# Optimization experiments

Measured on AMD Instinct MI355X. Metric: run time of the kernel, lower is better.

Reference implementation:

```python
import jax, jax.numpy as jnp
import numpy as np

B, T, N = 32, 64, 2048
HID, HEADS, DH, BOT, MAX_LAG = 256, 8, 32, 64, 7


def setup_inputs() -> dict:
    key = jax.random.key(0)
    ks = jax.random.split(key, 12)
    def nrm(k, shape, s=0.05):
        return jax.random.normal(k, shape, jnp.float32) * s
    # delay logits init as in the module: log(softmaxed exp decay)
    w = np.exp(-np.arange(MAX_LAG + 1) / 3.0)
    w = w / w.sum()
    delay_logits = jnp.asarray(np.log(w + 1e-8), jnp.float32)
    # row-normalized adjacency prior (done in __init__ of the module)
    adj_raw = jax.random.uniform(ks[0], (N, N), jnp.float32)
    adj_prior = adj_raw / (adj_raw.sum(-1, keepdims=True) + 1e-8)
    return {
        "x": jax.random.normal(ks[1], (B, T, N), jnp.float32),
        "features": jax.random.normal(ks[2], (B, N, HID), jnp.float32),
        "delay_logits": delay_logits,
        "w_dp": nrm(ks[3], (1, HID)), "b_dp": jnp.zeros((HID,), jnp.float32),
        "w_qkv_low": nrm(ks[4], (HID, 3 * BOT)), "b_qkv_low": jnp.zeros((3 * BOT,), jnp.float32),
        "w_qkv_high": nrm(ks[5], (3 * BOT, 3 * HID)), "b_qkv_high": jnp.zeros((3 * HID,), jnp.float32),
        "w_out_low": nrm(ks[6], (HID, BOT)), "b_out_low": jnp.zeros((BOT,), jnp.float32),
        "w_out_high": nrm(ks[7], (BOT, HID)), "b_out_high": jnp.zeros((HID,), jnp.float32),
        "adj_prior": adj_prior,
        "geo_weight": jnp.array([0.3], jnp.float32),
        "ln_gamma": jnp.ones((HID,), jnp.float32),
        "ln_beta": jnp.zeros((HID,), jnp.float32),
    }


def reference(x, features, delay_logits, w_dp, b_dp,
              w_qkv_low, b_qkv_low, w_qkv_high, b_qkv_high,
              w_out_low, b_out_low, w_out_high, b_out_high,
              adj_prior, geo_weight, ln_gamma, ln_beta):
    # --- delay-weighted signal (generation interval) ---
    dw = jax.nn.softmax(delay_logits)                      # [max_lag+1]
    taus = min(MAX_LAG + 1, T)                              # static
    x_lags = jnp.flip(x, axis=1)[:, :taus]                  # [B,taus,N], lag tau = x[:, -(tau+1)]
    delayed = jnp.einsum('t,btn->bn', dw[:taus], x_lags)    # [B,N]
    delay_feat = delayed[:, :, None] * w_dp[0] + b_dp       # Linear(1, hidden)
    combined = features + 0.1 * delay_feat                  # [B,N,HID]

    # --- low-rank QKV ---
    qkv = (combined @ w_qkv_low + b_qkv_low) @ w_qkv_high + b_qkv_high  # [B,N,3*HID]
    q, k, v = jnp.split(qkv, 3, axis=-1)
    def to_heads(t):
        return t.reshape(B, N, HEADS, DH).transpose(0, 2, 1, 3)  # [B,H,N,dh]
    q, k, v = to_heads(q), to_heads(k), to_heads(v)

    # --- linear attention (elu+1 feature map, O(N)) ---
    qf = jax.nn.elu(q) + 1.0
    kf = jax.nn.elu(k) + 1.0
    kv = jnp.einsum('bhnd,bhne->bhde', kf, v)               # [B,H,dh,dh]
    k_sum = kf.sum(axis=2) + 1e-8                           # [B,H,dh]
    num = jnp.einsum('bhnd,bhde->bhne', qf, kv)             # [B,H,N,dh]
    den = jnp.einsum('bhnd,bhd->bhn', qf, k_sum)[..., None] + 1e-8
    attended = num / den

    # --- geo-adjacency blend ---
    gb = jax.nn.sigmoid(geo_weight[0])
    v_geo = jnp.einsum('nm,bhmd->bhnd', adj_prior, v)       # dense graph mixing
    attended = (1.0 - gb) * attended + gb * v_geo

    attended = attended.transpose(0, 2, 1, 3).reshape(B, N, HID)
    # dropout is identity in eval mode
    out = (attended @ w_out_low + b_out_low) @ w_out_high + b_out_high

    # --- residual + LayerNorm ---
    y = out + features
    mu = y.mean(-1, keepdims=True)
    var = ((y - mu) ** 2).mean(-1, keepdims=True)
    return (y - mu) / jnp.sqrt(var + 1e-5) * ln_gamma + ln_beta
```

## Files before the change

kernel.cpp:

```cpp
#include <hip/hip_runtime.h>
#include <hip/hip_bf16.h>
#include <stdint.h>

typedef unsigned short u16;
typedef float f4v __attribute__((ext_vector_type(4)));
typedef short s8v __attribute__((ext_vector_type(8)));


__device__ __forceinline__ float bf2f(u16 u) {
  union { float f; uint32_t i; } x; x.i = ((uint32_t)u) << 16; return x.f;
}
__device__ __forceinline__ u16 f2bf(float f) {
  uint32_t u = __float_as_uint(f);
  u = (u + 0x7FFFu + ((u >> 16) & 1u)) >> 16;
  return (u16)u;
}
__device__ __forceinline__ uint32_t pk2(float a, float b) {
  return (uint32_t)f2bf(a) | ((uint32_t)f2bf(b) << 16);
}
__device__ __forceinline__ void gload16(const void* g, void* l) {
  __builtin_amdgcn_global_load_lds((const __attribute__((address_space(1))) void*)g,
                                   (__attribute__((address_space(3))) void*)l, 16, 0, 0);
}

__global__ __launch_bounds__(256) void prep_all_k(
    const float* __restrict__ x, const float* __restrict__ dlog,
    const float* __restrict__ w_dp, const float* __restrict__ b_dp,
    const float* __restrict__ wql, const float* __restrict__ bql,
    const float* __restrict__ wqh, const float* __restrict__ wol,
    const float* __restrict__ bqh,
    float* __restrict__ wl_d, float* __restrict__ bl_p, float* __restrict__ delayed,
    u16* __restrict__ wqlT, u16* __restrict__ wqhT, u16* __restrict__ wvlT,
    float* __restrict__ cvl) {
  const int bid = blockIdx.x, t = threadIdx.x;
  if (bid < 256) {
    float mx = dlog[0];
#pragma unroll
    for (int i = 1; i < 8; ++i) mx = fmaxf(mx, dlog[i]);
    float w8[8], ssum = 0.f;
#pragma unroll
    for (int i = 0; i < 8; ++i) { w8[i] = __expf(dlog[i] - mx); ssum += w8[i]; }
    float inv = 1.f / ssum;
    int r = bid * 256 + t;
    int b = r >> 11, n = r & 2047;
    const float* xb = x + (size_t)b * 64 * 2048;
    float acc = 0.f;
#pragma unroll
    for (int tau = 0; tau < 8; ++tau) acc += w8[tau] * inv * xb[(size_t)(63 - tau) * 2048 + n];
    delayed[r] = acc;
  } else if (bid < 512) {
    int n = bid - 256;
    wqlT[(size_t)n * 256 + t] = f2bf(n < 192 ? wql[(size_t)t * 192 + n] : 0.f);
  } else if (bid < 1280) {
    int n = bid - 512;
    if (t < 192) wqhT[(size_t)n * 192 + t] = f2bf(wqh[(size_t)t * 768 + n]);
  } else if (bid < 1408) {
    int d = bid - 1280;
    __shared__ float wolc[256];
    if (d < 64) wolc[t] = wol[(size_t)t * 64 + d];
    __syncthreads();
    if (t < 192) {
      float s = 0.f;
      if (d < 64) {
        const float* wr = wqh + (size_t)t * 768 + 512;
        for (int c = 0; c < 256; ++c) s = fmaf(wr[c], wolc[c], s);
      }
      wvlT[(size_t)d * 192 + t] = f2bf(s);
    }
    if (t == 0 && d < 64) {
      float s = 0.f;
      for (int c = 0; c < 256; ++c) s = fmaf(bqh[512 + c], wolc[c], s);
      cvl[d] = s;
    }
  } else {
    if (t < 192) {
      float s1 = 0.f, s2 = 0.f;
      for (int k = 0; k < 256; ++k) {
        float w = wql[k * 192 + t];
        s1 += w_dp[k] * w;
        s2 += b_dp[k] * w;
      }
      wl_d[t] = 0.1f * s1;
      bl_p[t] = bql[t] + 0.1f * s2;
    }
  }
}

struct MArgs {
  const u16* A;
  const float* Af32;
  const u16* Bt;
  const float* delayed; const float* wl_d; const float* bl_p;
  const float* bqh;
  const float* cvl;
  u16* low; u16* qf; u16* kf; u16* v; u16* vpt;
  u16* geopart;
};

enum { GLOW = 0, GQKV = 1, GGEO = 2, GVP = 3 };

template <int MODE>
__global__ __launch_bounds__(256) void mgemm_k(MArgs ma) {
  constexpr int KLOOP = (MODE == GLOW) ? 256 : (MODE == GQKV) ? 192 :
                        (MODE == GGEO) ? 512 : 192;
  constexpr int LDA = (MODE == GLOW) ? 256 : (MODE == GGEO) ? 2048 : 192;
  constexpr int LDB = (MODE == GLOW) ? 256 : (MODE == GGEO) ? 2048 : 192;

  __shared__ __align__(16) u16 Al[128 * 64];
  __shared__ __align__(16) u16 Bl[128 * 64];

  const int t = threadIdx.x;
  const int l = t & 63, w = t >> 6;
  const int wm = w >> 1, wn = w & 1;

  int ct, rt, bz = 0;
  if constexpr (MODE == GGEO) {
    int lin = blockIdx.x + 16 * blockIdx.y + 256 * blockIdx.z;
    int xcd = lin & 7, idx = lin >> 3;
    ct = idx & 15;
    int pid = xcd * 8 + (idx >> 4);
    rt = pid & 15;
    bz = pid >> 4;
  } else {
    constexpr int NCT = (MODE == GLOW) ? 2 : (MODE == GQKV) ? 6 : 1;
    int lin = blockIdx.x + NCT * blockIdx.y;
    int xcd = lin & 7, idx = lin >> 3;
    ct = idx % NCT; rt = xcd * 64 + idx / NCT;
  }
  const int kbase = (MODE == GGEO) ? bz * 512 : 0;

  f4v acc[4][4] = {};

  for (int k0 = 0; k0 < KLOOP; k0 += 64) {
    __syncthreads();
#pragma unroll
    for (int s = 0; s < 4; ++s) {
      int c = s * 256 + t;
      int r = c >> 3, cc = c & 7;
      int g = ((cc & 3) ^ ((r >> 1) & 3)) | ((cc & 4) ^ ((r & 1) << 2));
      int row = rt * 128 + r;
      int kg = kbase + k0 + g * 8;
      if constexpr (MODE == GLOW || MODE == GGEO) {
        const float* src = ma.Af32 + (size_t)row * LDA + kg;
        float4 x0 = *(const float4*)src;
        float4 x1 = *(const float4*)(src + 4);
        uint4 qq = {pk2(x0.x, x0.y), pk2(x0.z, x0.w), pk2(x1.x, x1.y), pk2(x1.z, x1.w)};
        *(uint4*)&Al[c * 8] = qq;
      } else {
        gload16(ma.A + (size_t)row * LDA + kg, (char*)Al + (s * 4 + w) * 1024);
      }
      gload16(ma.Bt + (size_t)(ct * 128 + r) * LDB + kg,
              (char*)Bl + (s * 4 + w) * 1024);
    }
    __syncthreads();

#pragma unroll
    for (int kk = 0; kk < 64; kk += 32) {
      s8v fa[4], fb[4];
#pragma unroll
      for (int mr = 0; mr < 4; ++mr) {
        int ra = wm * 64 + mr * 16 + (l & 15);
        int ch = ((l >> 4) ^ ((ra >> 1) & 3)) | ((kk >> 3) ^ ((ra & 1) << 2));
        fa[mr] = *(const s8v*)(Al + ra * 64 + ch * 8);
      }
#pragma unroll
      for (int nr = 0; nr < 4; ++nr) {
        int rb = wn * 64 + nr * 16 + (l & 15);
        int cb = ((l >> 4) ^ ((rb >> 1) & 3)) | ((kk >> 3) ^ ((rb & 1) << 2));
        fb[nr] = *(const s8v*)(Bl + rb * 64 + cb * 8);
      }
      if constexpr (MODE == GVP) {
#pragma unroll
        for (int mr = 0; mr < 4; ++mr)
#pragma unroll
          for (int nr = 0; nr < 4; ++nr)
            acc[mr][nr] = __builtin_amdgcn_mfma_f32_16x16x32_bf16(fa[mr], fb[nr], acc[mr][nr], 0, 0, 0);
      } else {
#pragma unroll
        for (int mr = 0; mr < 4; ++mr)
#pragma unroll
          for (int nr = 0; nr < 4; ++nr)
            acc[mr][nr] = __builtin_amdgcn_mfma_f32_16x16x32_bf16(fb[nr], fa[mr], acc[mr][nr], 0, 0, 0);
      }
    }
  }

  const int r0 = rt * 128 + wm * 64, c0 = ct * 128 + wn * 64;

  if constexpr (MODE == GVP) {
    const int lr = (l >> 4) * 4, lc = l & 15;
#pragma unroll
    for (int mr = 0; mr < 4; ++mr)
#pragma unroll
      for (int nr = 0; nr < 4; ++nr) {
        if (wn == 0) {
          int d = nr * 16 + lc;
          float cadd = ma.cvl[d];
          int n0 = (r0 + mr * 16 + lr) & 2047;
          int b = rt >> 4;
          ushort4 st = {f2bf(acc[mr][nr][0] + cadd), f2bf(acc[mr][nr][1] + cadd),
                        f2bf(acc[mr][nr][2] + cadd), f2bf(acc[mr][nr][3] + cadd)};
          *(ushort4*)(ma.vpt + ((size_t)(b * 64 + d)) * 2048 + n0) = st;
        }
      }
  } else {
    const int rowl = l & 15, colq = (l >> 4) * 4;
#pragma unroll
    for (int mr = 0; mr < 4; ++mr) {
      int row = r0 + mr * 16 + rowl;
#pragma unroll
      for (int nr = 0; nr < 4; ++nr) {
        int col0 = c0 + nr * 16 + colq;
        if constexpr (MODE == GLOW) {
          if (col0 < 192) {
            float dl = ma.delayed[row];
            float4 wd = *(const float4*)(ma.wl_d + col0);
            float4 bp = *(const float4*)(ma.bl_p + col0);
            ushort4 st = {f2bf(acc[mr][nr][0] + dl * wd.x + bp.x),
                          f2bf(acc[mr][nr][1] + dl * wd.y + bp.y),
                          f2bf(acc[mr][nr][2] + dl * wd.z + bp.z),
                          f2bf(acc[mr][nr][3] + dl * wd.w + bp.w)};
            *(ushort4*)(ma.low + (size_t)row * 192 + col0) = st;
          }
        } else if constexpr (MODE == GQKV) {
          int third = ct >> 1;
          int lc2 = col0 & 255;
          u16* dst = (third == 0) ? ma.qf : (third == 1 ? ma.kf : ma.v);
          float4 bias = *(const float4*)(ma.bqh + col0);
          float v0 = acc[mr][nr][0] + bias.x;
          float v1 = acc[mr][nr][1] + bias.y;
          float v2 = acc[mr][nr][2] + bias.z;
          float v3 = acc[mr][nr][3] + bias.w;
          if (third < 2) {
            v0 = (v0 > 0.f) ? (v0 + 1.f) : __expf(v0);
            v1 = (v1 > 0.f) ? (v1 + 1.f) : __expf(v1);
            v2 = (v2 > 0.f) ? (v2 + 1.f) : __expf(v2);
            v3 = (v3 > 0.f) ? (v3 + 1.f) : __expf(v3);
          }
          ushort4 st = {f2bf(v0), f2bf(v1), f2bf(v2), f2bf(v3)};
          *(ushort4*)(dst + (size_t)row * 256 + lc2) = st;
        } else {
          u16* dst = ma.geopart + (size_t)bz * 4194304;
          ushort4 st = {f2bf(acc[mr][nr][0]), f2bf(acc[mr][nr][1]),
                        f2bf(acc[mr][nr][2]), f2bf(acc[mr][nr][3])};
          *(ushort4*)(dst + (size_t)row * 2048 + col0) = st;
        }
      }
    }
  }
}

__global__ __launch_bounds__(256) void gfin_k(const u16* __restrict__ qf,
                                              const float* __restrict__ rden,
                                              const u16* __restrict__ geopart,
                                              const u16* __restrict__ B2t,
                                              const float* __restrict__ cvec,
                                              const float* __restrict__ feats,
                                              const float* __restrict__ gamma,
                                              const float* __restrict__ beta,
                                              float* __restrict__ y) {
  __shared__ __align__(16) u16 Al[64 * 32];
  __shared__ __align__(16) u16 Bl[256 * 32];
  __shared__ float LN1[4][64], LN2[4][64];

  const int t = threadIdx.x;
  const int l = t & 63, w = t >> 6;
  const int rt = blockIdx.x;
  const int b = rt >> 5;

  f4v acc[4][4] = {};

  for (int k0 = 0; k0 < 320; k0 += 32) {
    __syncthreads();
    {
      int c = t;
      int r = c >> 2, cc = c & 3;
      int g = cc ^ ((r >> 1) & 3);
      int row = rt * 64 + r;
      int kg = k0 + g * 8;
      if (k0 < 256) {
        float sc = rden[(size_t)row * 8 + (kg >> 5)];
        s8v qv = *(const s8v*)(qf + (size_t)row * 256 + kg);
        uint4 qq = {pk2(bf2f((u16)qv[0]) * sc, bf2f((u16)qv[1]) * sc),
                    pk2(bf2f((u16)qv[2]) * sc, bf2f((u16)qv[3]) * sc),
                    pk2(bf2f((u16)qv[4]) * sc, bf2f((u16)qv[5]) * sc),
                    pk2(bf2f((u16)qv[6]) * sc, bf2f((u16)qv[7]) * sc)};
        *(uint4*)&Al[c * 8] = qq;
      } else {
        int n = row & 2047;
        const u16* gp = geopart + (size_t)n * 2048 + b * 64 + (kg - 256);
        s8v p0 = *(const s8v*)(gp);
        s8v p1 = *(const s8v*)(gp + 4194304);
        s8v p2 = *(const s8v*)(gp + 8388608);
        s8v p3 = *(const s8v*)(gp + 12582912);
        float vv[8];
#pragma unroll
        for (int j = 0; j < 8; ++j)
          vv[j] = bf2f((u16)p0[j]) + bf2f((u16)p1[j]) + bf2f((u16)p2[j]) + bf2f((u16)p3[j]);
        uint4 qq = {pk2(vv[0], vv[1]), pk2(vv[2], vv[3]), pk2(vv[4], vv[5]), pk2(vv[6], vv[7])};
        *(uint4*)&Al[c * 8] = qq;
      }
    }
#pragma unroll
    for (int s = 0; s < 4; ++s) {
      int c = s * 256 + t;
      int r = c >> 2, cc = c & 3;
      int g = cc ^ ((r >> 1) & 3);
      gload16(B2t + ((size_t)b * 256 + r) * 320 + k0 + g * 8,
              (char*)Bl + (s * 4 + w) * 1024);
    }
    __syncthreads();

    s8v fa[4], fb[4];
#pragma unroll
    for (int mr = 0; mr < 4; ++mr) {
      int ra = mr * 16 + (l & 15);
      int ca = (l >> 4) ^ ((ra >> 1) & 3);
      fa[mr] = *(const s8v*)(Al + ra * 32 + ca * 8);
    }
#pragma unroll
    for (int nr = 0; nr < 4; ++nr) {
      int rb = w * 64 + nr * 16 + (l & 15);
      int cb = (l >> 4) ^ ((rb >> 1) & 3);
      fb[nr] = *(const s8v*)(Bl + rb * 32 + cb * 8);
    }
#pragma unroll
    for (int mr = 0; mr < 4; ++mr)
#pragma unroll
      for (int nr = 0; nr < 4; ++nr)
        acc[mr][nr] = __builtin_amdgcn_mfma_f32_16x16x32_bf16(fb[nr], fa[mr], acc[mr][nr], 0, 0, 0);
  }

  const int rowl = l & 15, colq = (l >> 4) * 4;
  float s1v[4] = {0.f, 0.f, 0.f, 0.f}, s2v[4] = {0.f, 0.f, 0.f, 0.f};
#pragma unroll
  for (int mr = 0; mr < 4; ++mr) {
    int row = rt * 64 + mr * 16 + rowl;
#pragma unroll
    for (int nr = 0; nr < 4; ++nr) {
      int col0 = w * 64 + nr * 16 + colq;
      float4 cv = *(const float4*)(cvec + col0);
      float4 ft = *(const float4*)(feats + (size_t)row * 256 + col0);
      f4v vv = acc[mr][nr];
      vv[0] += cv.x + ft.x; vv[1] += cv.y + ft.y;
      vv[2] += cv.z + ft.z; vv[3] += cv.w + ft.w;
      acc[mr][nr] = vv;
      s1v[mr] += vv[0] + vv[1] + vv[2] + vv[3];
      s2v[mr] += vv[0] * vv[0] + vv[1] * vv[1] + vv[2] * vv[2] + vv[3] * vv[3];
    }
  }
#pragma unroll
  for (int mr = 0; mr < 4; ++mr) {
    s1v[mr] += __shfl_xor(s1v[mr], 16); s2v[mr] += __shfl_xor(s2v[mr], 16);
    s1v[mr] += __shfl_xor(s1v[mr], 32); s2v[mr] += __shfl_xor(s2v[mr], 32);
  }
  if (l < 16) {
#pragma unroll
    for (int mr = 0; mr < 4; ++mr) {
      LN1[w][mr * 16 + l] = s1v[mr];
      LN2[w][mr * 16 + l] = s2v[mr];
    }
  }
  __syncthreads();
#pragma unroll
  for (int mr = 0; mr < 4; ++mr) {
    int rl = mr * 16 + rowl;
    int row = rt * 64 + rl;
    float s1 = LN1[0][rl] + LN1[1][rl] + LN1[2][rl] + LN1[3][rl];
    float s2 = LN2[0][rl] + LN2[1][rl] + LN2[2][rl] + LN2[3][rl];
    float mu = s1 * (1.f / 256.f);
    float var = s2 * (1.f / 256.f) - mu * mu;
    float rstd = rsqrtf(fmaxf(var, 0.f) + 1e-5f);
#pragma unroll
    for (int nr = 0; nr < 4; ++nr) {
      int col0 = w * 64 + nr * 16 + colq;
      float4 g4 = *(const float4*)(gamma + col0);
      float4 b4 = *(const float4*)(beta + col0);
      f4v vv = acc[mr][nr];
      float4 o;
      o.x = (vv[0] - mu) * rstd * g4.x + b4.x;
      o.y = (vv[1] - mu) * rstd * g4.y + b4.y;
      o.z = (vv[2] - mu) * rstd * g4.z + b4.z;
      o.w = (vv[3] - mu) * rstd * g4.w + b4.w;
      *(float4*)(y + (size_t)row * 256 + col0) = o;
    }
  }
}

__global__ __launch_bounds__(256) void kvreduce_k(const u16* __restrict__ kf,
                                                  const u16* __restrict__ v,
                                                  u16* __restrict__ kvpart,
                                                  float* __restrict__ kspart) {
  const int chunk = blockIdx.x, h = blockIdx.y, b = blockIdx.z;
  const int t = threadIdx.x, w = t >> 6, lane = t & 63;
  __shared__ float kfs[64][32], vs[64][32];
  const int d0 = (lane >> 3) * 4, e0 = (lane & 7) * 4;
  float acc[4][4] = {};
  float ks[4] = {0.f, 0.f, 0.f, 0.f};
  const int row0 = chunk * 1024;
  const int rr = t >> 2, c8 = (t & 3) * 8;
  for (int it = 0; it < 16; ++it) {
    __syncthreads();
    size_t g = ((size_t)(b * 2048 + row0 + it * 64 + rr)) * 256 + h * 32 + c8;
    s8v ku = *(const s8v*)(kf + g);
    s8v vu = *(const s8v*)(v + g);
#pragma unroll
    for (int j = 0; j < 8; ++j) {
      kfs[rr][c8 + j] = bf2f((u16)ku[j]);
      vs[rr][c8 + j] = bf2f((u16)vu[j]);
    }
    __syncthreads();
#pragma unroll
    for (int ri = 0; ri < 16; ++ri) {
      int r = w * 16 + ri;
      float4 a = *(const float4*)&kfs[r][d0];
      float4 bb = *(const float4*)&vs[r][e0];
      float aa[4] = {a.x, a.y, a.z, a.w};
      float bbv[4] = {bb.x, bb.y, bb.z, bb.w};
#pragma unroll
      for (int i = 0; i < 4; ++i)
#pragma unroll
        for (int j = 0; j < 4; ++j) acc[i][j] = fmaf(aa[i], bbv[j], acc[i][j]);
      if (e0 == 0) {
        ks[0] += aa[0]; ks[1] += aa[1]; ks[2] += aa[2]; ks[3] += aa[3];
      }
    }
  }
  const int p = chunk * 4 + w;
  u16* kvp = kvpart + ((size_t)p * 256 + b * 8 + h) * 1024;
#pragma unroll
  for (int i = 0; i < 4; ++i)
#pragma unroll
    for (int j = 0; j < 4; ++j) kvp[(d0 + i) * 32 + e0 + j] = f2bf(acc[i][j]);
  if (e0 == 0) {
    float* ksp = kspart + ((size_t)p * 256 + b * 8 + h) * 32;
#pragma unroll
    for (int i = 0; i < 4; ++i) ksp[d0 + i] = ks[i];
  }
}

__global__ __launch_bounds__(64) void mmat_k(const u16* __restrict__ kvpart,
                                             const float* __restrict__ wol,
                                             const float* __restrict__ geow,
                                             float* __restrict__ Mm) {
  const int bh = blockIdx.x;
  const int h = bh & 7, b = bh >> 3;
  const int c = threadIdx.x;
  __shared__ float kvs[32][32];
  for (int i = c; i < 1024; i += 64) {
    float s = 0.f;
#pragma unroll
    for (int p = 0; p < 8; ++p) s += bf2f(kvpart[(size_t)(p * 256 + bh) * 1024 + i]);
    kvs[i >> 5][i & 31] = s;
  }
  __syncthreads();
  float one_m = 1.f - 1.f / (1.f + __expf(-geow[0]));
  float acc[32];
#pragma unroll
  for (int d = 0; d < 32; ++d) acc[d] = 0.f;
  for (int e = 0; e < 32; ++e) {
    float w = wol[(size_t)(h * 32 + e) * 64 + c];
#pragma unroll
    for (int d = 0; d < 32; ++d) acc[d] = fmaf(kvs[d][e], w, acc[d]);
  }
  float* mp = Mm + (size_t)b * 16384 + (size_t)h * 32 * 64 + c;
#pragma unroll
  for (int d = 0; d < 32; ++d) mp[d * 64] = one_m * acc[d];
}

__global__ __launch_bounds__(256) void bprep_k(const float* __restrict__ Mm,
                                               const float* __restrict__ woh,
                                               const float* __restrict__ bol,
                                               const float* __restrict__ boh,
                                               const float* __restrict__ geow,
                                               u16* __restrict__ B2t,
                                               float* __restrict__ cvec) {
  const int kt = blockIdx.x, b = blockIdx.y;
  const int c = threadIdx.x;
  __shared__ float Ms[64][64];
#pragma unroll
  for (int i = 0; i < 16; ++i) {
    int flat = c + i * 256;
    int kk = flat >> 6, e = flat & 63;
    Ms[kk][e] = Mm[(size_t)b * 16384 + (size_t)(kt * 64 + kk) * 64 + e];
  }
  __syncthreads();
  float wcol[64];
#pragma unroll
  for (int e = 0; e < 64; ++e) wcol[e] = woh[(size_t)e * 256 + c];
  u16* dst = B2t + ((size_t)b * 256 + c) * 320;
  for (int kk = 0; kk < 64; ++kk) {
    float s = 0.f;
#pragma unroll
    for (int e = 0; e < 64; ++e) s = fmaf(Ms[kk][e], wcol[e], s);
    dst[kt * 64 + kk] = f2bf(s);
  }
  if (kt == 0) {
    float gb = 1.f / (1.f + __expf(-geow[0]));
#pragma unroll
    for (int d = 0; d < 64; ++d) dst[256 + d] = f2bf(gb * wcol[d]);
    if (b == 0) {
      float s = boh[c];
#pragma unroll
      for (int d = 0; d < 64; ++d) s = fmaf(bol[d], wcol[d], s);
      cvec[c] = s;
    }
  }
}

__global__ __launch_bounds__(256) void rden_k(const u16* __restrict__ qf,
                                              const float* __restrict__ kspart,
                                              float* __restrict__ rden) {
  const int t = threadIdx.x;
  const int b = (blockIdx.x * 16) >> 11;
  __shared__ float ksumf[256];
  {
    int h = t >> 5, e = t & 31;
    float s = 0.f;
#pragma unroll
    for (int p = 0; p < 8; ++p) s += kspart[(size_t)(p * 256 + b * 8 + h) * 32 + e];
    ksumf[t] = s + 1e-8f;
  }
  __syncthreads();
  const int row = blockIdx.x * 16 + (t >> 4);
  const int c0 = (t & 15) * 16;
  s8v q0 = *(const s8v*)(qf + (size_t)row * 256 + c0);
  s8v q1 = *(const s8v*)(qf + (size_t)row * 256 + c0 + 8);
  float part = 0.f;
#pragma unroll
  for (int j = 0; j < 8; ++j) part = fmaf(bf2f((u16)q0[j]), ksumf[c0 + j], part);
#pragma unroll
  for (int j = 0; j < 8; ++j) part = fmaf(bf2f((u16)q1[j]), ksumf[c0 + 8 + j], part);
  float den = part + __shfl_xor(part, 1);
  if ((t & 1) == 0) rden[(size_t)row * 8 + (c0 >> 5)] = 1.f / (den + 1e-8f);
}

extern "C" void kernel_launch(void* const* d_in, const int* in_sizes, int n_in,
                              void* d_out, int out_size, void* d_ws, size_t ws_size,
                              hipStream_t stream) {
  const float* x     = (const float*)d_in[0];
  const float* feats = (const float*)d_in[1];
  const float* dlog  = (const float*)d_in[2];
  const float* w_dp  = (const float*)d_in[3];
  const float* b_dp  = (const float*)d_in[4];
  const float* wql   = (const float*)d_in[5];
  const float* bql   = (const float*)d_in[6];
  const float* wqh   = (const float*)d_in[7];
  const float* bqh   = (const float*)d_in[8];
  const float* wol   = (const float*)d_in[9];
  const float* bol   = (const float*)d_in[10];
  const float* woh   = (const float*)d_in[11];
  const float* boh   = (const float*)d_in[12];
  const float* adj   = (const float*)d_in[13];
  const float* geow  = (const float*)d_in[14];
  const float* gamma = (const float*)d_in[15];
  const float* beta  = (const float*)d_in[16];

  char* ws = (char*)d_ws;
  constexpr size_t OFF_WLD   = 1024;
  constexpr size_t OFF_BLP   = 2048;
  constexpr size_t OFF_CVEC  = 4096;
  constexpr size_t OFF_CVL   = 5120;
  constexpr size_t OFF_DEL   = 8192;
  constexpr size_t OFF_WQLT  = 270336;
  constexpr size_t OFF_WQHT  = 401408;
  constexpr size_t OFF_WVLT  = 696320;
  constexpr size_t OFF_KSP   = 745472;
  constexpr size_t OFF_RDEN  = 1007616;
  constexpr size_t OFF_MM    = 3104768;
  constexpr size_t OFF_B2T   = 5201920;
  constexpr size_t OFF_KVP   = OFF_B2T;
  constexpr size_t OFF_LOW   = 10444800;
  constexpr size_t OFF_QF    = 35610624;
  constexpr size_t OFF_KF    = 69165056;
  constexpr size_t OFF_VPT   = OFF_KF;
  constexpr size_t OFF_V     = 102719488;
  constexpr size_t OFF_GPART = OFF_V;

  float* wl_d    = (float*)(ws + OFF_WLD);
  float* bl_p    = (float*)(ws + OFF_BLP);
  float* cvec    = (float*)(ws + OFF_CVEC);
  float* cvl     = (float*)(ws + OFF_CVL);
  float* delayed = (float*)(ws + OFF_DEL);
  float* kspart  = (float*)(ws + OFF_KSP);
  float* rden    = (float*)(ws + OFF_RDEN);
  float* Mm      = (float*)(ws + OFF_MM);
  u16* kvpart = (u16*)(ws + OFF_KVP);
  u16* wqlT = (u16*)(ws + OFF_WQLT);
  u16* wqhT = (u16*)(ws + OFF_WQHT);
  u16* wvlT = (u16*)(ws + OFF_WVLT);
  u16* B2t  = (u16*)(ws + OFF_B2T);

  MArgs ma{};
  ma.delayed = delayed; ma.wl_d = wl_d; ma.bl_p = bl_p; ma.bqh = bqh; ma.cvl = cvl;
  ma.low = (u16*)(ws + OFF_LOW);
  ma.qf  = (u16*)(ws + OFF_QF);
  ma.kf  = (u16*)(ws + OFF_KF);
  ma.v   = (u16*)(ws + OFF_V);
  ma.vpt = (u16*)(ws + OFF_VPT);
  ma.geopart = (u16*)(ws + OFF_GPART);

  prep_all_k<<<1409, 256, 0, stream>>>(x, dlog, w_dp, b_dp, wql, bql, wqh, wol, bqh,
                                       wl_d, bl_p, delayed, wqlT, wqhT, wvlT, cvl);

  MArgs m0 = ma; m0.Af32 = feats; m0.Bt = wqlT;
  mgemm_k<GLOW><<<dim3(2, 512), 256, 0, stream>>>(m0);

  MArgs m1 = ma; m1.A = ma.low; m1.Bt = wqhT;
  mgemm_k<GQKV><<<dim3(6, 512), 256, 0, stream>>>(m1);

  kvreduce_k<<<dim3(2, 8, 32), 256, 0, stream>>>(ma.kf, ma.v, kvpart, kspart);
  mmat_k<<<256, 64, 0, stream>>>(kvpart, wol, geow, Mm);
  bprep_k<<<dim3(4, 32), 256, 0, stream>>>(Mm, woh, bol, boh, geow, B2t, cvec);
  rden_k<<<4096, 256, 0, stream>>>(ma.qf, kspart, rden);

  MArgs m2 = ma; m2.A = ma.low; m2.Bt = wvlT;
  mgemm_k<GVP><<<dim3(1, 512), 256, 0, stream>>>(m2);

  MArgs m3 = ma; m3.Af32 = adj; m3.Bt = ma.vpt;
  mgemm_k<GGEO><<<dim3(16, 16, 4), 256, 0, stream>>>(m3);

  gfin_k<<<1024, 256, 0, stream>>>(ma.qf, rden, ma.geopart, B2t, cvec,
                                   feats, gamma, beta, (float*)d_out);
  (void)in_sizes; (void)n_in; (void)out_size; (void)ws_size;
}
```

Baseline: 286.0 us.

## Split QKV GEMM, store K/V transposed, and reduce KV with MFMA

The fused QKV projection GEMM is split into a Q GEMM and a separate K/V GEMM. The K/V GEMM writes kf and v transposed (feature-major over N), so a new kvred_k kernel can compute the per-head K^T V products with bf16 MFMA straight from global memory. This replaces the scalar FMA reduction that staged data through LDS, and it writes fp32 partials over 4 chunks instead of bf16 partials over 8. The final gfin_k GEMM also moves from a K-step of 32 to 64 with a wider LDS swizzle, which halves the number of barrier iterations. The cost is one extra kernel launch, strided transposed stores in the K/V epilogue, and larger LDS use in gfin_k.

```diff
diff --git a/kernel.cpp b/kernel.cpp
--- a/kernel.cpp
+++ b/kernel.cpp
@@ -97,14 +97,14 @@
   u16* geopart;
 };
 
-enum { GLOW = 0, GQKV = 1, GGEO = 2, GVP = 3 };
+enum { GLOW = 0, GQ = 1, GKV = 2, GGEO = 3, GVP = 4 };
 
 template <int MODE>
 __global__ __launch_bounds__(256) void mgemm_k(MArgs ma) {
-  constexpr int KLOOP = (MODE == GLOW) ? 256 : (MODE == GQKV) ? 192 :
-                        (MODE == GGEO) ? 512 : 192;
+  constexpr int KLOOP = (MODE == GLOW) ? 256 : (MODE == GGEO) ? 512 : 192;
   constexpr int LDA = (MODE == GLOW) ? 256 : (MODE == GGEO) ? 2048 : 192;
   constexpr int LDB = (MODE == GLOW) ? 256 : (MODE == GGEO) ? 2048 : 192;
+  constexpr bool SWAPPED = (MODE == GLOW || MODE == GQ || MODE == GGEO);
 
   __shared__ __align__(16) u16 Al[128 * 64];
   __shared__ __align__(16) u16 Bl[128 * 64];
@@ -122,7 +122,7 @@
     rt = pid & 15;
     bz = pid >> 4;
   } else {
-    constexpr int NCT = (MODE == GLOW) ? 2 : (MODE == GQKV) ? 6 : 1;
+    constexpr int NCT = (MODE == GLOW || MODE == GQ) ? 2 : (MODE == GKV) ? 4 : 1;
     int lin = blockIdx.x + NCT * blockIdx.y;
     int xcd = lin & 7, idx = lin >> 3;
     ct = idx % NCT; rt = xcd * 64 + idx / NCT;
@@ -169,18 +169,18 @@
         int cb = ((l >> 4) ^ ((rb >> 1) & 3)) | ((kk >> 3) ^ ((rb & 1) << 2));
         fb[nr] = *(const s8v*)(Bl + rb * 64 + cb * 8);
       }
-      if constexpr (MODE == GVP) {
+      if constexpr (SWAPPED) {
+#pragma unroll
+        for (int mr = 0; mr < 4; ++mr)
+#pragma unroll
+          for (int nr = 0; nr < 4; ++nr)
+            acc[mr][nr] = __builtin_amdgcn_mfma_f32_16x16x32_bf16(fb[nr], fa[mr], acc[mr][nr], 0, 0, 0);
+      } else {
 #pragma unroll
         for (int mr = 0; mr < 4; ++mr)
 #pragma unroll
           for (int nr = 0; nr < 4; ++nr)
             acc[mr][nr] = __builtin_amdgcn_mfma_f32_16x16x32_bf16(fa[mr], fb[nr], acc[mr][nr], 0, 0, 0);
-      } else {
-#pragma unroll
-        for (int mr = 0; mr < 4; ++mr)
-#pragma unroll
-          for (int nr = 0; nr < 4; ++nr)
-            acc[mr][nr] = __builtin_amdgcn_mfma_f32_16x16x32_bf16(fb[nr], fa[mr], acc[mr][nr], 0, 0, 0);
       }
     }
   }
@@ -202,6 +202,33 @@
                         f2bf(acc[mr][nr][2] + cadd), f2bf(acc[mr][nr][3] + cadd)};
           *(ushort4*)(ma.vpt + ((size_t)(b * 64 + d)) * 2048 + n0) = st;
         }
+      }
+  } else if constexpr (MODE == GKV) {
+    const int lr = (l >> 4) * 4, lc = l & 15;
+#pragma unroll
+    for (int mr = 0; mr < 4; ++mr)
+#pragma unroll
+      for (int nr = 0; nr < 4; ++nr) {
+        int chat = ct * 128 + wn * 64 + nr * 16 + lc;
+        float bias = ma.bqh[256 + chat];
+        int n0 = (r0 + mr * 16 + lr) & 2047;
+        int b = rt >> 4;
+        float v0 = acc[mr][nr][0] + bias;
+        float v1 = acc[mr][nr][1] + bias;
+        float v2 = acc[mr][nr][2] + bias;
+        float v3 = acc[mr][nr][3] + bias;
+        u16* dst;
+        if (chat < 256) {
+          v0 = (v0 > 0.f) ? (v0 + 1.f) : __expf(v0);
+          v1 = (v1 > 0.f) ? (v1 + 1.f) : __expf(v1);
+          v2 = (v2 > 0.f) ? (v2 + 1.f) : __expf(v2);
+          v3 = (v3 > 0.f) ? (v3 + 1.f) : __expf(v3);
+          dst = ma.kf + ((size_t)(b * 256 + chat)) * 2048;
+        } else {
+          dst = ma.v + ((size_t)(b * 256 + chat - 256)) * 2048;
+        }
+        ushort4 st = {f2bf(v0), f2bf(v1), f2bf(v2), f2bf(v3)};
+        *(ushort4*)(dst + n0) = st;
       }
   } else {
     const int rowl = l & 15, colq = (l >> 4) * 4;
@@ -222,23 +249,18 @@
                           f2bf(acc[mr][nr][3] + dl * wd.w + bp.w)};
             *(ushort4*)(ma.low + (size_t)row * 192 + col0) = st;
           }
-        } else if constexpr (MODE == GQKV) {
-          int third = ct >> 1;
-          int lc2 = col0 & 255;
-          u16* dst = (third == 0) ? ma.qf : (third == 1 ? ma.kf : ma.v);
+        } else if constexpr (MODE == GQ) {
           float4 bias = *(const float4*)(ma.bqh + col0);
           float v0 = acc[mr][nr][0] + bias.x;
           float v1 = acc[mr][nr][1] + bias.y;
           float v2 = acc[mr][nr][2] + bias.z;
           float v3 = acc[mr][nr][3] + bias.w;
-          if (third < 2) {
-            v0 = (v0 > 0.f) ? (v0 + 1.f) : __expf(v0);
-            v1 = (v1 > 0.f) ? (v1 + 1.f) : __expf(v1);
-            v2 = (v2 > 0.f) ? (v2 + 1.f) : __expf(v2);
-            v3 = (v3 > 0.f) ? (v3 + 1.f) : __expf(v3);
-          }
+          v0 = (v0 > 0.f) ? (v0 + 1.f) : __expf(v0);
+          v1 = (v1 > 0.f) ? (v1 + 1.f) : __expf(v1);
+          v2 = (v2 > 0.f) ? (v2 + 1.f) : __expf(v2);
+          v3 = (v3 > 0.f) ? (v3 + 1.f) : __expf(v3);
           ushort4 st = {f2bf(v0), f2bf(v1), f2bf(v2), f2bf(v3)};
-          *(ushort4*)(dst + (size_t)row * 256 + lc2) = st;
+          *(ushort4*)(ma.qf + (size_t)row * 256 + col0) = st;
         } else {
           u16* dst = ma.geopart + (size_t)bz * 4194304;
           ushort4 st = {f2bf(acc[mr][nr][0]), f2bf(acc[mr][nr][1]),
@@ -248,6 +270,66 @@
       }
     }
   }
+}
+
+__global__ __launch_bounds__(256) void kvred_k(const u16* __restrict__ kfT,
+                                               const u16* __restrict__ vT,
+                                               float* __restrict__ kvpart,
+                                               float* __restrict__ kspart) {
+  const int z = blockIdx.x, h = blockIdx.y, b = blockIdx.z;
+  const int t = threadIdx.x, l = t & 63, w = t >> 6;
+  const size_t base = ((size_t)(b * 256 + h * 32)) * 2048 + z * 512 + w * 128;
+  const u16* ka = kfT + base;
+  const u16* vb = vT + base;
+  f4v acc[2][2] = {};
+  float ks[2] = {0.f, 0.f};
+#pragma unroll
+  for (int s = 0; s < 4; ++s) {
+    int koff = s * 32 + (l >> 4) * 8;
+    s8v fa[2], fb[2];
+#pragma unroll
+    for (int mr = 0; mr < 2; ++mr)
+      fa[mr] = *(const s8v*)(ka + (size_t)(mr * 16 + (l & 15)) * 2048 + koff);
+#pragma unroll
+    for (int nr = 0; nr < 2; ++nr)
+      fb[nr] = *(const s8v*)(vb + (size_t)(nr * 16 + (l & 15)) * 2048 + koff);
+#pragma unroll
+    for (int mr = 0; mr < 2; ++mr) {
+      float sacc = 0.f;
+#pragma unroll
+      for (int j = 0; j < 8; ++j) sacc += bf2f((u16)fa[mr][j]);
+      ks[mr] += sacc;
+    }
+#pragma unroll
+    for (int mr = 0; mr < 2; ++mr)
+#pragma unroll
+      for (int nr = 0; nr < 2; ++nr)
+        acc[mr][nr] = __builtin_amdgcn_mfma_f32_16x16x32_bf16(fa[mr], fb[nr], acc[mr][nr], 0, 0, 0);
+  }
+  ks[0] += __shfl_xor(ks[0], 16); ks[0] += __shfl_xor(ks[0], 32);
+  ks[1] += __shfl_xor(ks[1], 16); ks[1] += __shfl_xor(ks[1], 32);
+
+  __shared__ float kvs[4][32][32];
+  __shared__ float kss[4][32];
+#pragma unroll
+  for (int mr = 0; mr < 2; ++mr)
+#pragma unroll
+    for (int nr = 0; nr < 2; ++nr)
+#pragma unroll
+      for (int i = 0; i < 4; ++i)
+        kvs[w][mr * 16 + (l >> 4) * 4 + i][nr * 16 + (l & 15)] = acc[mr][nr][i];
+  if (l < 16) { kss[w][l] = ks[0]; kss[w][16 + l] = ks[1]; }
+  __syncthreads();
+  float* kvp = kvpart + ((size_t)(z * 256 + b * 8 + h)) * 1024;
+#pragma unroll
+  for (int q = 0; q < 4; ++q) {
+    int idx = q * 256 + t;
+    kvp[idx] = kvs[0][idx >> 5][idx & 31] + kvs[1][idx >> 5][idx & 31] +
+               kvs[2][idx >> 5][idx & 31] + kvs[3][idx >> 5][idx & 31];
+  }
+  if (t < 32)
+    kspart[((size_t)(z * 256 + b * 8 + h)) * 32 + t] =
+        kss[0][t] + kss[1][t] + kss[2][t] + kss[3][t];
 }
 
 __global__ __launch_bounds__(256) void gfin_k(const u16* __restrict__ qf,
@@ -259,8 +341,8 @@
                                               const float* __restrict__ gamma,
                                               const float* __restrict__ beta,
                                               float* __restrict__ y) {
-  __shared__ __align__(16) u16 Al[64 * 32];
-  __shared__ __align__(16) u16 Bl[256 * 32];
+  __shared__ __align__(16) u16 Al[64 * 64];
+  __shared__ __align__(16) u16 Bl[256 * 64];
   __shared__ float LN1[4][64], LN2[4][64];
 
   const int t = threadIdx.x;
@@ -270,12 +352,13 @@
 
   f4v acc[4][4] = {};
 
-  for (int k0 = 0; k0 < 320; k0 += 32) {
+  for (int k0 = 0; k0 < 320; k0 += 64) {
     __syncthreads();
-    {
-      int c = t;
-      int r = c >> 2, cc = c & 3;
-      int g = cc ^ ((r >> 1) & 3);
+#pragma unroll
+    for (int s = 0; s < 2; ++s) {
+      int c = s * 256 + t;
+      int r = c >> 3, cc = c & 7;
+      int g = ((cc & 3) ^ ((r >> 1) & 3)) | ((cc & 4) ^ ((r & 1) << 2));
       int row = rt * 64 + r;
       int kg = k0 + g * 8;
       if (k0 < 256) {
@@ -302,33 +385,36 @@
       }
     }
 #pragma unroll
-    for (int s = 0; s < 4; ++s) {
+    for (int s = 0; s < 8; ++s) {
       int c = s * 256 + t;
-      int r = c >> 2, cc = c & 3;
-      int g = cc ^ ((r >> 1) & 3);
+      int r = c >> 3, cc = c & 7;
+      int g = ((cc & 3) ^ ((r >> 1) & 3)) | ((cc & 4) ^ ((r & 1) << 2));
       gload16(B2t + ((size_t)b * 256 + r) * 320 + k0 + g * 8,
               (char*)Bl + (s * 4 + w) * 1024);
     }
     __syncthreads();
 
-    s8v fa[4], fb[4];
-#pragma unroll
-    for (int mr = 0; mr < 4; ++mr) {
-      int ra = mr * 16 + (l & 15);
-      int ca = (l >> 4) ^ ((ra >> 1) & 3);
-      fa[mr] = *(const s8v*)(Al + ra * 32 + ca * 8);
-    }
-#pragma unroll
-    for (int nr = 0; nr < 4; ++nr) {
-      int rb = w * 64 + nr * 16 + (l & 15);
-      int cb = (l >> 4) ^ ((rb >> 1) & 3);
-      fb[nr] = *(const s8v*)(Bl + rb * 32 + cb * 8);
-    }
-#pragma unroll
-    for (int mr = 0; mr < 4; ++mr)
-#pragma unroll
-      for (int nr = 0; nr < 4; ++nr)
-        acc[mr][nr] = __builtin_amdgcn_mfma_f32_16x16x32_bf16(fb[nr], fa[mr], acc[mr][nr], 0, 0, 0);
+#pragma unroll
+    for (int kk = 0; kk < 64; kk += 32) {
+      s8v fa[4], fb[4];
+#pragma unroll
+      for (int mr = 0; mr < 4; ++mr) {
+        int ra = mr * 16 + (l & 15);
+        int ch = ((l >> 4) ^ ((ra >> 1) & 3)) | ((kk >> 3) ^ ((ra & 1) << 2));
+        fa[mr] = *(const s8v*)(Al + ra * 64 + ch * 8);
+      }
+#pragma unroll
+      for (int nr = 0; nr < 4; ++nr) {
+        int rb = w * 64 + nr * 16 + (l & 15);
+        int cb = ((l >> 4) ^ ((rb >> 1) & 3)) | ((kk >> 3) ^ ((rb & 1) << 2));
+        fb[nr] = *(const s8v*)(Bl + rb * 64 + cb * 8);
+      }
+#pragma unroll
+      for (int mr = 0; mr < 4; ++mr)
+#pragma unroll
+        for (int nr = 0; nr < 4; ++nr)
+          acc[mr][nr] = __builtin_amdgcn_mfma_f32_16x16x32_bf16(fb[nr], fa[mr], acc[mr][nr], 0, 0, 0);
+    }
   }
 
   const int rowl = l & 15, colq = (l >> 4) * 4;
@@ -387,59 +473,7 @@
   }
 }
 
-__global__ __launch_bounds__(256) void kvreduce_k(const u16* __restrict__ kf,
-                                                  const u16* __restrict__ v,
-                                                  u16* __restrict__ kvpart,
-                                                  float* __restrict__ kspart) {
-  const int chunk = blockIdx.x, h = blockIdx.y, b = blockIdx.z;
-  const int t = threadIdx.x, w = t >> 6, lane = t & 63;
-  __shared__ float kfs[64][32], vs[64][32];
-  const int d0 = (lane >> 3) * 4, e0 = (lane & 7) * 4;
-  float acc[4][4] = {};
-  float ks[4] = {0.f, 0.f, 0.f, 0.f};
-  const int row0 = chunk * 1024;
-  const int rr = t >> 2, c8 = (t & 3) * 8;
-  for (int it = 0; it < 16; ++it) {
-    __syncthreads();
-    size_t g = ((size_t)(b * 2048 + row0 + it * 64 + rr)) * 256 + h * 32 + c8;
-    s8v ku = *(const s8v*)(kf + g);
-    s8v vu = *(const s8v*)(v + g);
-#pragma unroll
-    for (int j = 0; j < 8; ++j) {
-      kfs[rr][c8 + j] = bf2f((u16)ku[j]);
-      vs[rr][c8 + j] = bf2f((u16)vu[j]);
-    }
-    __syncthreads();
-#pragma unroll
-    for (int ri = 0; ri < 16; ++ri) {
-      int r = w * 16 + ri;
-      float4 a = *(const float4*)&kfs[r][d0];
-      float4 bb = *(const float4*)&vs[r][e0];
-      float aa[4] = {a.x, a.y, a.z, a.w};
-      float bbv[4] = {bb.x, bb.y, bb.z, bb.w};
-#pragma unroll
-      for (int i = 0; i < 4; ++i)
-#pragma unroll
-        for (int j = 0; j < 4; ++j) acc[i][j] = fmaf(aa[i], bbv[j], acc[i][j]);
-      if (e0 == 0) {
-        ks[0] += aa[0]; ks[1] += aa[1]; ks[2] += aa[2]; ks[3] += aa[3];
-      }
-    }
-  }
-  const int p = chunk * 4 + w;
-  u16* kvp = kvpart + ((size_t)p * 256 + b * 8 + h) * 1024;
-#pragma unroll
-  for (int i = 0; i < 4; ++i)
-#pragma unroll
-    for (int j = 0; j < 4; ++j) kvp[(d0 + i) * 32 + e0 + j] = f2bf(acc[i][j]);
-  if (e0 == 0) {
-    float* ksp = kspart + ((size_t)p * 256 + b * 8 + h) * 32;
-#pragma unroll
-    for (int i = 0; i < 4; ++i) ksp[d0 + i] = ks[i];
-  }
-}
-
-__global__ __launch_bounds__(64) void mmat_k(const u16* __restrict__ kvpart,
+__global__ __launch_bounds__(64) void mmat_k(const float* __restrict__ kvpart,
                                              const float* __restrict__ wol,
                                              const float* __restrict__ geow,
                                              float* __restrict__ Mm) {
@@ -450,7 +484,7 @@
   for (int i = c; i < 1024; i += 64) {
     float s = 0.f;
 #pragma unroll
-    for (int p = 0; p < 8; ++p) s += bf2f(kvpart[(size_t)(p * 256 + bh) * 1024 + i]);
+    for (int p = 0; p < 4; ++p) s += kvpart[(size_t)(p * 256 + bh) * 1024 + i];
     kvs[i >> 5][i & 31] = s;
   }
   __syncthreads();
@@ -518,7 +552,7 @@
     int h = t >> 5, e = t & 31;
     float s = 0.f;
 #pragma unroll
-    for (int p = 0; p < 8; ++p) s += kspart[(size_t)(p * 256 + b * 8 + h) * 32 + e];
+    for (int p = 0; p < 4; ++p) s += kspart[(size_t)(p * 256 + b * 8 + h) * 32 + e];
     ksumf[t] = s + 1e-8f;
   }
   __syncthreads();
@@ -566,9 +600,9 @@
   constexpr size_t OFF_WQHT  = 401408;
   constexpr size_t OFF_WVLT  = 696320;
   constexpr size_t OFF_KSP   = 745472;
-  constexpr size_t OFF_RDEN  = 1007616;
-  constexpr size_t OFF_MM    = 3104768;
-  constexpr size_t OFF_B2T   = 5201920;
+  constexpr size_t OFF_RDEN  = 876544;
+  constexpr size_t OFF_MM    = 2973696;
+  constexpr size_t OFF_B2T   = 5070848;
   constexpr size_t OFF_KVP   = OFF_B2T;
   constexpr size_t OFF_LOW   = 10444800;
   constexpr size_t OFF_QF    = 35610624;
@@ -585,7 +619,7 @@
   float* kspart  = (float*)(ws + OFF_KSP);
   float* rden    = (float*)(ws + OFF_RDEN);
   float* Mm      = (float*)(ws + OFF_MM);
-  u16* kvpart = (u16*)(ws + OFF_KVP);
+  float* kvpart  = (float*)(ws + OFF_KVP);
   u16* wqlT = (u16*)(ws + OFF_WQLT);
   u16* wqhT = (u16*)(ws + OFF_WQHT);
   u16* wvlT = (u16*)(ws + OFF_WVLT);
@@ -607,12 +641,15 @@
   mgemm_k<GLOW><<<dim3(2, 512), 256, 0, stream>>>(m0);
 
   MArgs m1 = ma; m1.A = ma.low; m1.Bt = wqhT;
-  mgemm_k<GQKV><<<dim3(6, 512), 256, 0, stream>>>(m1);
-
-  kvreduce_k<<<dim3(2, 8, 32), 256, 0, stream>>>(ma.kf, ma.v, kvpart, kspart);
+  mgemm_k<GQ><<<dim3(2, 512), 256, 0, stream>>>(m1);
+
+  MArgs m1b = ma; m1b.A = ma.low; m1b.Bt = wqhT + (size_t)256 * 192;
+  mgemm_k<GKV><<<dim3(4, 512), 256, 0, stream>>>(m1b);
+
+  kvred_k<<<dim3(4, 8, 32), 256, 0, stream>>>(ma.kf, ma.v, kvpart, kspart);
   mmat_k<<<256, 64, 0, stream>>>(kvpart, wol, geow, Mm);
+  rden_k<<<4096, 256, 0, stream>>>(ma.qf, kspart, rden);
   bprep_k<<<dim3(4, 32), 256, 0, stream>>>(Mm, woh, bol, boh, geow, B2t, cvec);
-  rden_k<<<4096, 256, 0, stream>>>(ma.qf, kspart, rden);
 
   MArgs m2 = ma; m2.A = ma.low; m2.Bt = wvlT;
   mgemm_k<GVP><<<dim3(1, 512), 256, 0, stream>>>(m2);
```

Result: faster. 279.2 us (-2.4%).
